# Kernel tuning notes

Measured on AMD Instinct MI355X. Metric: run time of the kernel, lower is better.

## Reference

```python
import jax, jax.numpy as jnp
import numpy as np


def setup_inputs() -> dict:
    key = jax.random.key(0)
    k1, k2, k3, k4 = jax.random.split(key, 4)
    B, N_LEAVES, D_IN, L, C = 64, 512, 512, 5, 4
    n_nodes = 2 * N_LEAVES - 1  # heap layout: node i has children 2i+1, 2i+2
    h = jax.random.normal(k1, (B, n_nodes, D_IN), dtype=jnp.float32)
    W = jax.random.normal(k2, (D_IN, L * C), dtype=jnp.float32) * (1.0 / np.sqrt(D_IN))
    b = jax.random.normal(k3, (L * C,), dtype=jnp.float32) * 0.02
    trans = jax.random.normal(k4, (L, L, L, C, C, C), dtype=jnp.float32) * 0.1
    return {"h": h, "W": W, "b": b, "trans": trans}


def reference(h, W, b, trans):
    """Batched inside algorithm of BinaryTreeLatentVariable.forward.

    h: [B, n_nodes, D] node hidden states (complete binary tree, heap order).
    Returns root inside score [B, L, C].
    """
    B, n_nodes, _ = h.shape
    L = trans.shape[0]
    C = trans.shape[3]
    n_leaves = (n_nodes + 1) // 2
    depth = int(np.log2(n_leaves))

    # Emission: state_weight_layer applied to every node at once.
    sw = (h @ W + b).reshape(B, n_nodes, L, C)  # [B, N, L, C]

    # Leaves: in_weight = state_weight. Internal slots overwritten bottom-up.
    in_w = sw
    for d in range(depth - 1, -1, -1):  # level-synchronous, bottom-up
        start, end = 2 ** d - 1, 2 ** (d + 1) - 1  # internal nodes of this level
        l = in_w[:, 2 * start + 1:2 * end:2]        # [B, m, L, C] left children
        r = in_w[:, 2 * start + 2:2 * end + 1:2]    # [B, m, L, C] right children
        p = sw[:, start:end]                        # [B, m, L, C] parent emission
        # score[b,m, pL,lL,rL, pc,lc,rc]
        score = (p[:, :, :, None, None, :, None, None]
                 + l[:, :, None, :, None, None, :, None]
                 + r[:, :, None, None, :, None, None, :]
                 + trans)
        new = jax.nn.logsumexp(score, axis=(3, 4, 6, 7))  # marginalize children
        in_w = in_w.at[:, start:end].set(new)
    return in_w[:, 0]  # root inside score [B, L, C]
```

## Files before the change

### kernel.cpp

```cpp
#include <hip/hip_runtime.h>
#include <hip/hip_bf16.h>
#include <math.h>

#define NB      64
#define NNODES  1023
#define LC      20
#define DIN     512
#define NROWS   (NB * NNODES)
#define ET_PAD  404

#define BM      128
#define BK      64
#define NKC     (DIN / BK)
#define SCP     21

typedef unsigned short u16;
typedef short bf16x8 __attribute__((ext_vector_type(8)));
typedef float f32x4  __attribute__((ext_vector_type(4)));

__device__ __forceinline__ u16 f2bf(float f) {
    unsigned x = __float_as_uint(f);
    return (u16)((x + 0x7FFFu + ((x >> 16) & 1u)) >> 16);
}

__global__ __launch_bounds__(256) void prep_kernel(
    const float* __restrict__ trans, const float* __restrict__ W,
    float* __restrict__ ET, u16* __restrict__ Bfrag)
{
    int t = blockIdx.x * 256 + threadIdx.x;
    if (t < 8000) {
        int q   = t % 20;
        int rem = t / 20;
        int j   = rem % 20;
        int i   = rem / 20;
        int ll = i >> 2, cl = i & 3;
        int lr = j >> 2, cr = j & 3;
        int lp = q >> 2, cp = q & 3;
        int src = ((((lp * 5 + ll) * 5 + lr) * 4 + cp) * 4 + cl) * 4 + cr;
        ET[q * ET_PAD + i * 20 + j] = expf(trans[src]);
    }
    if (t < 2048) {
        int lane = t & 63, nf = (t >> 6) & 1, ks = t >> 7;
        int col = nf * 16 + (lane & 15);
        int kb  = ks * 32 + (lane >> 4) * 8;
        unsigned e[8];
        #pragma unroll
        for (int j = 0; j < 8; ++j)
            e[j] = (col < LC) ? (unsigned)f2bf(W[(kb + j) * LC + col]) : 0u;
        uint4 v;
        v.x = e[0] | (e[1] << 16); v.y = e[2] | (e[3] << 16);
        v.z = e[4] | (e[5] << 16); v.w = e[6] | (e[7] << 16);
        ((uint4*)Bfrag)[t] = v;
    }
}

__global__ __launch_bounds__(256, 2) void gemm_kernel(
    const float* __restrict__ h, const u16* __restrict__ Bfrag,
    const float* __restrict__ bias, float* __restrict__ buf)
{
    __shared__ u16 AsU[2][BM][64];
    __shared__ u16 BsU[2048 * 8];
    const int t    = threadIdx.x;
    const int lane = t & 63;
    const int wv   = t >> 6;
    const size_t row0 = (size_t)blockIdx.x * BM;

    {
        const uint4* s = (const uint4*)Bfrag;
        uint4* d = (uint4*)BsU;
        #pragma unroll
        for (int i = 0; i < 8; ++i) d[t + 256 * i] = s[t + 256 * i];
    }

    const int srow = t >> 4;
    const int sk4  = t & 15;
    const int woff = (((sk4 >> 1) ^ (srow & 7)) << 3) + ((sk4 & 1) << 2);
    const float* hp[8];
    #pragma unroll
    for (int i = 0; i < 8; ++i) {
        size_t gr = row0 + srow + 16 * i;
        if (gr >= NROWS) gr = NROWS - 1;
        hp[i] = h + gr * DIN + sk4 * 4;
    }

    f32x4 acc00 = {0.f,0.f,0.f,0.f}, acc01 = {0.f,0.f,0.f,0.f};
    f32x4 acc10 = {0.f,0.f,0.f,0.f}, acc11 = {0.f,0.f,0.f,0.f};
    float4 R0[8], R1[8], R2[8];

#define ISSUE(RB, CC) { _Pragma("unroll")                                     \
    for (int i = 0; i < 8; ++i) RB[i] = *(const float4*)(hp[i] + (CC) * BK); }

#define CVTWRITE(RB, P) { u16* _b = &AsU[P][0][0] + woff; _Pragma("unroll")   \
    for (int i = 0; i < 8; ++i) {                                             \
        uint2 pk;                                                             \
        pk.x = (unsigned)f2bf(RB[i].x) | ((unsigned)f2bf(RB[i].y) << 16);     \
        pk.y = (unsigned)f2bf(RB[i].z) | ((unsigned)f2bf(RB[i].w) << 16);     \
        *(uint2*)(_b + (srow + 16 * i) * 64) = pk; } }

#define COMPUTE(P, C) { const u16* _ab = &AsU[P][0][0]; _Pragma("unroll")     \
    for (int kc = 0; kc < 2; ++kc) {                                          \
        int rsl = (((kc * 4 + (lane >> 4)) ^ (lane & 7)) << 3);               \
        bf16x8 a0 = *(const bf16x8*)(_ab + (wv*32      + (lane&15))*64 + rsl);\
        bf16x8 a1 = *(const bf16x8*)(_ab + (wv*32 + 16 + (lane&15))*64 + rsl);\
        const u16* _bb = &BsU[(((C)*2 + kc) * 2 * 64 + lane) * 8];            \
        bf16x8 b0 = *(const bf16x8*)(_bb);                                    \
        bf16x8 b1 = *(const bf16x8*)(_bb + 64 * 8);                           \
        acc00 = __builtin_amdgcn_mfma_f32_16x16x32_bf16(a0, b0, acc00, 0,0,0);\
        acc01 = __builtin_amdgcn_mfma_f32_16x16x32_bf16(a0, b1, acc01, 0,0,0);\
        acc10 = __builtin_amdgcn_mfma_f32_16x16x32_bf16(a1, b0, acc10, 0,0,0);\
        acc11 = __builtin_amdgcn_mfma_f32_16x16x32_bf16(a1, b1, acc11, 0,0,0);\
    } }

    ISSUE(R0, 0); ISSUE(R1, 1); ISSUE(R2, 2);
    CVTWRITE(R0, 0);
    __syncthreads();

    #pragma unroll
    for (int c = 0; c < NKC; ++c) {
        if (c + 3 < NKC) {
            if ((c % 3) == 0)      { ISSUE(R0, c + 3); }
            else if ((c % 3) == 1) { ISSUE(R1, c + 3); }
            else                   { ISSUE(R2, c + 3); }
        }
        COMPUTE(c & 1, c);
        if (c + 1 < NKC) {
            if (((c + 1) % 3) == 0)      { CVTWRITE(R0, (c + 1) & 1); }
            else if (((c + 1) % 3) == 1) { CVTWRITE(R1, (c + 1) & 1); }
            else                         { CVTWRITE(R2, (c + 1) & 1); }
        }
        __syncthreads();
    }
#undef ISSUE
#undef CVTWRITE
#undef COMPUTE

    float* sc = (float*)&AsU[0][0][0];
    #pragma unroll
    for (int mf = 0; mf < 2; ++mf) {
        #pragma unroll
        for (int nf = 0; nf < 2; ++nf) {
            f32x4 a = (mf == 0) ? (nf == 0 ? acc00 : acc01)
                                : (nf == 0 ? acc10 : acc11);
            int col = nf * 16 + (lane & 15);
            if (col < LC) {
                float bv = bias[col];
                #pragma unroll
                for (int p = 0; p < 4; ++p) {
                    int rl = wv * 32 + mf * 16 + (lane >> 4) * 4 + p;
                    sc[rl * SCP + col] = a[p] + bv;
                }
            }
        }
    }
    __syncthreads();
    {
        const size_t rem = NROWS - row0;
        const int vmax = (int)((rem < BM ? rem : (size_t)BM) * 5);
        #pragma unroll
        for (int i = 0; i < 3; ++i) {
            int p = t + 256 * i;
            if (p < 640 && p < vmax) {
                int f0 = p * 4;
                float4 o;
                o.x = sc[((f0 + 0) / 20) * SCP + (f0 + 0) % 20];
                o.y = sc[((f0 + 1) / 20) * SCP + (f0 + 1) % 20];
                o.z = sc[((f0 + 2) / 20) * SCP + (f0 + 2) % 20];
                o.w = sc[((f0 + 3) / 20) * SCP + (f0 + 3) % 20];
                ((float4*)(buf + row0 * LC))[p] = o;
            }
        }
    }
}

__device__ __forceinline__ void level_body(
    float* __restrict__ buf, const float* __restrict__ et,
    float* __restrict__ out, int bi, int node, int q)
{
    size_t pbase = ((size_t)bi * NNODES + node) * LC;
    size_t lbase = ((size_t)bi * NNODES + 2 * node + 1) * LC;

    float l[LC], r[LC];
    const float4* l4 = (const float4*)(buf + lbase);
    const float4* r4 = (const float4*)(buf + lbase + LC);
    #pragma unroll
    for (int v = 0; v < 5; ++v) {
        float4 lv = l4[v], rv = r4[v];
        l[4*v+0] = lv.x; l[4*v+1] = lv.y; l[4*v+2] = lv.z; l[4*v+3] = lv.w;
        r[4*v+0] = rv.x; r[4*v+1] = rv.y; r[4*v+2] = rv.z; r[4*v+3] = rv.w;
    }
    float maxl = l[0], maxr = r[0];
    #pragma unroll
    for (int i = 1; i < LC; ++i) {
        maxl = fmaxf(maxl, l[i]);
        maxr = fmaxf(maxr, r[i]);
    }
    float el[LC], er[LC];
    #pragma unroll
    for (int i = 0; i < LC; ++i) {
        el[i] = __expf(l[i] - maxl);
        er[i] = __expf(r[i] - maxr);
    }

    const float4* etq = (const float4*)(et + q * ET_PAD);
    float s = 0.f;
    #pragma unroll
    for (int i = 0; i < LC; ++i) {
        float4 e0 = etq[i*5+0], e1 = etq[i*5+1], e2 = etq[i*5+2],
               e3 = etq[i*5+3], e4 = etq[i*5+4];
        float d0 = 0.f, d1 = 0.f;
        d0 = fmaf(e0.x, er[0],  d0); d1 = fmaf(e0.y, er[1],  d1);
        d0 = fmaf(e0.z, er[2],  d0); d1 = fmaf(e0.w, er[3],  d1);
        d0 = fmaf(e1.x, er[4],  d0); d1 = fmaf(e1.y, er[5],  d1);
        d0 = fmaf(e1.z, er[6],  d0); d1 = fmaf(e1.w, er[7],  d1);
        d0 = fmaf(e2.x, er[8],  d0); d1 = fmaf(e2.y, er[9],  d1);
        d0 = fmaf(e2.z, er[10], d0); d1 = fmaf(e2.w, er[11], d1);
        d0 = fmaf(e3.x, er[12], d0); d1 = fmaf(e3.y, er[13], d1);
        d0 = fmaf(e3.z, er[14], d0); d1 = fmaf(e3.w, er[15], d1);
        d0 = fmaf(e4.x, er[16], d0); d1 = fmaf(e4.y, er[17], d1);
        d0 = fmaf(e4.z, er[18], d0); d1 = fmaf(e4.w, er[19], d1);
        s = fmaf(el[i], d0 + d1, s);
    }

    float val = buf[pbase + q] + maxl + maxr + __logf(s);
    buf[pbase + q] = val;
    if (out) out[(size_t)bi * LC + q] = val;
}

__global__ __launch_bounds__(256) void level_kernel(
    float* __restrict__ buf, const float* __restrict__ ETg,
    int start, int count)
{
    __shared__ float et[LC * ET_PAD];
    for (int idx = threadIdx.x; idx < LC * ET_PAD / 4; idx += 256)
        ((float4*)et)[idx] = ((const float4*)ETg)[idx];
    __syncthreads();

    int t  = blockIdx.x * 256 + threadIdx.x;
    int pj = t / LC;
    int q  = t - pj * LC;
    if (pj >= NB * count) return;
    int bi   = pj / count;
    int node = start + (pj - bi * count);
    level_body(buf, et, nullptr, bi, node, q);
}

__global__ __launch_bounds__(640) void tail_kernel(
    float* __restrict__ buf, const float* __restrict__ ETg,
    float* __restrict__ out)
{
    __shared__ float et[LC * ET_PAD];
    for (int idx = threadIdx.x; idx < LC * ET_PAD / 4; idx += 640)
        ((float4*)et)[idx] = ((const float4*)ETg)[idx];
    __syncthreads();

    const int bi = blockIdx.x;
    for (int d = 5; d >= 0; --d) {
        int count = 1 << d;
        int start = count - 1;
        int t = threadIdx.x;
        if (t < count * LC) {
            int node = start + t / LC;
            int q    = t % LC;
            level_body(buf, et, (d == 0) ? out : nullptr, bi, node, q);
        }
        __syncthreads();
    }
}

extern "C" void kernel_launch(void* const* d_in, const int* in_sizes, int n_in,
                              void* d_out, int out_size, void* d_ws, size_t ws_size,
                              hipStream_t stream)
{
    const float* h     = (const float*)d_in[0];
    const float* W     = (const float*)d_in[1];
    const float* bias  = (const float*)d_in[2];
    const float* trans = (const float*)d_in[3];

    char* ws = (char*)d_ws;
    float* ET    = (float*)(ws);
    u16*   Bfrag = (u16*)(ws + 32768);
    float* buf   = (float*)(ws + 65536);

    prep_kernel<<<32, 256, 0, stream>>>(trans, W, ET, Bfrag);

    gemm_kernel<<<(NROWS + BM - 1) / BM, 256, 0, stream>>>(h, Bfrag, bias, buf);

    for (int d = 8; d >= 6; --d) {
        int count = 1 << d;
        int start = count - 1;
        int T = NB * count * LC;
        level_kernel<<<(T + 255) / 256, 256, 0, stream>>>(buf, ET, start, count);
    }
    tail_kernel<<<NB, 640, 0, stream>>>(buf, ET, (float*)d_out);
}
```

Baseline: 71.23 us.

## Shrink GEMM tile, read B fragments from global, fold level 6 into tail

The GEMM block tile drops from 128 to 64 rows with occupancy hint 4, so each wave now computes a single 16-row fragment. The W fragments are loaded per k-step straight from global (cache) instead of being staged in LDS, which frees shared memory for more resident blocks. The k-loop is fully unrolled by hand, with barriers that wait only on LDS counters. Bounds clamping is removed because NROWS is an exact multiple of 64. The tail kernel now also processes tree level 6 by looping over 640-thread chunks, which removes one level_kernel launch at the cost of less parallelism for that level.

Result: no change. 71.85 us (+0.9%).

```diff
diff --git a/kernel.cpp b/kernel.cpp
--- a/kernel.cpp
+++ b/kernel.cpp
@@ -9,7 +9,7 @@
 #define NROWS   (NB * NNODES)
 #define ET_PAD  404
 
-#define BM      128
+#define BM      64
 #define BK      64
 #define NKC     (DIN / BK)
 #define SCP     21
@@ -54,120 +54,109 @@
     }
 }
 
-__global__ __launch_bounds__(256, 2) void gemm_kernel(
+__global__ __launch_bounds__(256, 4) void gemm_kernel(
     const float* __restrict__ h, const u16* __restrict__ Bfrag,
     const float* __restrict__ bias, float* __restrict__ buf)
 {
     __shared__ u16 AsU[2][BM][64];
-    __shared__ u16 BsU[2048 * 8];
     const int t    = threadIdx.x;
     const int lane = t & 63;
     const int wv   = t >> 6;
     const size_t row0 = (size_t)blockIdx.x * BM;
 
-    {
-        const uint4* s = (const uint4*)Bfrag;
-        uint4* d = (uint4*)BsU;
-        #pragma unroll
-        for (int i = 0; i < 8; ++i) d[t + 256 * i] = s[t + 256 * i];
-    }
-
     const int srow = t >> 4;
     const int sk4  = t & 15;
     const int woff = (((sk4 >> 1) ^ (srow & 7)) << 3) + ((sk4 & 1) << 2);
-    const float* hp[8];
-    #pragma unroll
-    for (int i = 0; i < 8; ++i) {
-        size_t gr = row0 + srow + 16 * i;
-        if (gr >= NROWS) gr = NROWS - 1;
-        hp[i] = h + gr * DIN + sk4 * 4;
-    }
+    const float* hp0 = h + (row0 + srow) * DIN + sk4 * 4;
+    const float* hp1 = hp0 + 16 * DIN;
+    const float* hp2 = hp0 + 32 * DIN;
+    const float* hp3 = hp0 + 48 * DIN;
 
     f32x4 acc00 = {0.f,0.f,0.f,0.f}, acc01 = {0.f,0.f,0.f,0.f};
-    f32x4 acc10 = {0.f,0.f,0.f,0.f}, acc11 = {0.f,0.f,0.f,0.f};
-    float4 R0[8], R1[8], R2[8];
-
-#define ISSUE(RB, CC) { _Pragma("unroll")                                     \
-    for (int i = 0; i < 8; ++i) RB[i] = *(const float4*)(hp[i] + (CC) * BK); }
+    float4 R0[4], R1[4], R2[4];
+
+#define ISSUE(RB, CC) {                                                       \
+    RB[0] = *(const float4*)(hp0 + (CC) * BK);                                \
+    RB[1] = *(const float4*)(hp1 + (CC) * BK);                                \
+    RB[2] = *(const float4*)(hp2 + (CC) * BK);                                \
+    RB[3] = *(const float4*)(hp3 + (CC) * BK); }
 
 #define CVTWRITE(RB, P) { u16* _b = &AsU[P][0][0] + woff; _Pragma("unroll")   \
-    for (int i = 0; i < 8; ++i) {                                             \
+    for (int i = 0; i < 4; ++i) {                                             \
         uint2 pk;                                                             \
         pk.x = (unsigned)f2bf(RB[i].x) | ((unsigned)f2bf(RB[i].y) << 16);     \
         pk.y = (unsigned)f2bf(RB[i].z) | ((unsigned)f2bf(RB[i].w) << 16);     \
         *(uint2*)(_b + (srow + 16 * i) * 64) = pk; } }
 
-#define COMPUTE(P, C) { const u16* _ab = &AsU[P][0][0]; _Pragma("unroll")     \
-    for (int kc = 0; kc < 2; ++kc) {                                          \
-        int rsl = (((kc * 4 + (lane >> 4)) ^ (lane & 7)) << 3);               \
-        bf16x8 a0 = *(const bf16x8*)(_ab + (wv*32      + (lane&15))*64 + rsl);\
-        bf16x8 a1 = *(const bf16x8*)(_ab + (wv*32 + 16 + (lane&15))*64 + rsl);\
-        const u16* _bb = &BsU[(((C)*2 + kc) * 2 * 64 + lane) * 8];            \
-        bf16x8 b0 = *(const bf16x8*)(_bb);                                    \
-        bf16x8 b1 = *(const bf16x8*)(_bb + 64 * 8);                           \
-        acc00 = __builtin_amdgcn_mfma_f32_16x16x32_bf16(a0, b0, acc00, 0,0,0);\
-        acc01 = __builtin_amdgcn_mfma_f32_16x16x32_bf16(a0, b1, acc01, 0,0,0);\
-        acc10 = __builtin_amdgcn_mfma_f32_16x16x32_bf16(a1, b0, acc10, 0,0,0);\
-        acc11 = __builtin_amdgcn_mfma_f32_16x16x32_bf16(a1, b1, acc11, 0,0,0);\
-    } }
+#define BCOMP(P, C) {                                                         \
+    const uint4* _bp = (const uint4*)Bfrag + (size_t)(C) * 256 + lane;        \
+    uint4 _f0 = _bp[0];   uint4 _f1 = _bp[64];                                \
+    uint4 _f2 = _bp[128]; uint4 _f3 = _bp[192];                               \
+    const u16* _ab = &AsU[P][0][0] + (wv * 16 + (lane & 15)) * 64;            \
+    int _r0 = (((lane >> 4)    ) ^ (lane & 7)) << 3;                          \
+    int _r1 = (((lane >> 4) + 4) ^ (lane & 7)) << 3;                          \
+    bf16x8 _a0 = *(const bf16x8*)(_ab + _r0);                                 \
+    bf16x8 _a1 = *(const bf16x8*)(_ab + _r1);                                 \
+    acc00 = __builtin_amdgcn_mfma_f32_16x16x32_bf16(                          \
+        _a0, __builtin_bit_cast(bf16x8, _f0), acc00, 0, 0, 0);                \
+    acc01 = __builtin_amdgcn_mfma_f32_16x16x32_bf16(                          \
+        _a0, __builtin_bit_cast(bf16x8, _f1), acc01, 0, 0, 0);                \
+    acc00 = __builtin_amdgcn_mfma_f32_16x16x32_bf16(                          \
+        _a1, __builtin_bit_cast(bf16x8, _f2), acc00, 0, 0, 0);                \
+    acc01 = __builtin_amdgcn_mfma_f32_16x16x32_bf16(                          \
+        _a1, __builtin_bit_cast(bf16x8, _f3), acc01, 0, 0, 0); }
+
+#define BAR() { asm volatile("s_waitcnt lgkmcnt(0)" ::: "memory");            \
+                __builtin_amdgcn_s_barrier(); }
 
     ISSUE(R0, 0); ISSUE(R1, 1); ISSUE(R2, 2);
     CVTWRITE(R0, 0);
-    __syncthreads();
-
-    #pragma unroll
-    for (int c = 0; c < NKC; ++c) {
-        if (c + 3 < NKC) {
-            if ((c % 3) == 0)      { ISSUE(R0, c + 3); }
-            else if ((c % 3) == 1) { ISSUE(R1, c + 3); }
-            else                   { ISSUE(R2, c + 3); }
-        }
-        COMPUTE(c & 1, c);
-        if (c + 1 < NKC) {
-            if (((c + 1) % 3) == 0)      { CVTWRITE(R0, (c + 1) & 1); }
-            else if (((c + 1) % 3) == 1) { CVTWRITE(R1, (c + 1) & 1); }
-            else                         { CVTWRITE(R2, (c + 1) & 1); }
-        }
-        __syncthreads();
-    }
+    BAR();
+    BCOMP(0, 0); ISSUE(R0, 3); CVTWRITE(R1, 1); BAR();
+    BCOMP(1, 1); ISSUE(R1, 4); CVTWRITE(R2, 0); BAR();
+    BCOMP(0, 2); ISSUE(R2, 5); CVTWRITE(R0, 1); BAR();
+    BCOMP(1, 3); ISSUE(R0, 6); CVTWRITE(R1, 0); BAR();
+    BCOMP(0, 4); ISSUE(R1, 7); CVTWRITE(R2, 1); BAR();
+    BCOMP(1, 5);               CVTWRITE(R0, 0); BAR();
+    BCOMP(0, 6);               CVTWRITE(R1, 1); BAR();
+    BCOMP(1, 7);
 #undef ISSUE
 #undef CVTWRITE
-#undef COMPUTE
+#undef BCOMP
+#undef BAR
 
     float* sc = (float*)&AsU[0][0][0];
     #pragma unroll
-    for (int mf = 0; mf < 2; ++mf) {
-        #pragma unroll
-        for (int nf = 0; nf < 2; ++nf) {
-            f32x4 a = (mf == 0) ? (nf == 0 ? acc00 : acc01)
-                                : (nf == 0 ? acc10 : acc11);
-            int col = nf * 16 + (lane & 15);
-            if (col < LC) {
-                float bv = bias[col];
-                #pragma unroll
-                for (int p = 0; p < 4; ++p) {
-                    int rl = wv * 32 + mf * 16 + (lane >> 4) * 4 + p;
-                    sc[rl * SCP + col] = a[p] + bv;
-                }
+    for (int nf = 0; nf < 2; ++nf) {
+        f32x4 a = nf ? acc01 : acc00;
+        int col = nf * 16 + (lane & 15);
+        if (col < LC) {
+            float bv = bias[col];
+            #pragma unroll
+            for (int p = 0; p < 4; ++p) {
+                int rl = wv * 16 + (lane >> 4) * 4 + p;
+                sc[rl * SCP + col] = a[p] + bv;
             }
         }
     }
     __syncthreads();
     {
-        const size_t rem = NROWS - row0;
-        const int vmax = (int)((rem < BM ? rem : (size_t)BM) * 5);
-        #pragma unroll
-        for (int i = 0; i < 3; ++i) {
-            int p = t + 256 * i;
-            if (p < 640 && p < vmax) {
-                int f0 = p * 4;
-                float4 o;
-                o.x = sc[((f0 + 0) / 20) * SCP + (f0 + 0) % 20];
-                o.y = sc[((f0 + 1) / 20) * SCP + (f0 + 1) % 20];
-                o.z = sc[((f0 + 2) / 20) * SCP + (f0 + 2) % 20];
-                o.w = sc[((f0 + 3) / 20) * SCP + (f0 + 3) % 20];
-                ((float4*)(buf + row0 * LC))[p] = o;
-            }
+        float4* dst = (float4*)(buf + row0 * LC);
+        int f0 = t * 4;
+        float4 o;
+        o.x = sc[((f0 + 0) / 20) * SCP + (f0 + 0) % 20];
+        o.y = sc[((f0 + 1) / 20) * SCP + (f0 + 1) % 20];
+        o.z = sc[((f0 + 2) / 20) * SCP + (f0 + 2) % 20];
+        o.w = sc[((f0 + 3) / 20) * SCP + (f0 + 3) % 20];
+        dst[t] = o;
+        if (t < 64) {
+            int p = 256 + t, g0 = p * 4;
+            float4 o2;
+            o2.x = sc[((g0 + 0) / 20) * SCP + (g0 + 0) % 20];
+            o2.y = sc[((g0 + 1) / 20) * SCP + (g0 + 1) % 20];
+            o2.z = sc[((g0 + 2) / 20) * SCP + (g0 + 2) % 20];
+            o2.w = sc[((g0 + 3) / 20) * SCP + (g0 + 3) % 20];
+            dst[p] = o2;
         }
     }
 }
@@ -254,14 +243,17 @@
     __syncthreads();
 
     const int bi = blockIdx.x;
-    for (int d = 5; d >= 0; --d) {
+    for (int d = 6; d >= 0; --d) {
         int count = 1 << d;
         int start = count - 1;
-        int t = threadIdx.x;
-        if (t < count * LC) {
-            int node = start + t / LC;
-            int q    = t % LC;
-            level_body(buf, et, (d == 0) ? out : nullptr, bi, node, q);
+        int total = count * LC;
+        for (int base = 0; base < total; base += 640) {
+            int idx = base + (int)threadIdx.x;
+            if (idx < total) {
+                int node = start + idx / LC;
+                int q    = idx % LC;
+                level_body(buf, et, (d == 0) ? out : nullptr, bi, node, q);
+            }
         }
         __syncthreads();
     }
@@ -283,9 +275,9 @@
 
     prep_kernel<<<32, 256, 0, stream>>>(trans, W, ET, Bfrag);
 
-    gemm_kernel<<<(NROWS + BM - 1) / BM, 256, 0, stream>>>(h, Bfrag, bias, buf);
-
-    for (int d = 8; d >= 6; --d) {
+    gemm_kernel<<<NROWS / BM, 256, 0, stream>>>(h, Bfrag, bias, buf);
+
+    for (int d = 8; d >= 7; --d) {
         int count = 1 << d;
         int start = count - 1;
         int T = NB * count * LC;
```
